# Optimization experiments

Measured on AMD Instinct MI355X. Metric: run time of the kernel, lower is better.

The kernel has to match this reference:

```python
import jax, jax.numpy as jnp
import numpy as np

N = 100000      # nodes
E = 1600000     # edges (avg degree 16)
IN_DIM = 128
OUT_DIM = 64


def setup_inputs() -> dict:
    key = jax.random.key(0)
    k0, k1, k2, k3, k4 = jax.random.split(key, 5)
    h = jax.random.normal(k0, (N, IN_DIM), dtype=jnp.float32)
    src = jax.random.randint(k1, (E,), 0, N)
    dst = jax.random.randint(k2, (E,), 0, N)
    W = jax.random.normal(k3, (OUT_DIM, IN_DIM), dtype=jnp.float32) * 0.05  # fc.weight
    a = jax.random.normal(k4, (2 * OUT_DIM,), dtype=jnp.float32) * 0.05     # attn_fc.weight (flattened)
    return {"h": h, "src": src, "dst": dst, "W": W, "a": a}


def reference(h, src, dst, W, a):
    # z = fc(h)
    z = h @ W.T                                   # [N, OUT_DIM]
    # attn_fc([z_src, z_dst]) == z_src @ a[:D] + z_dst @ a[D:]  (exact linear split)
    s_src = z @ a[:OUT_DIM]                       # [N]
    s_dst = z @ a[OUT_DIM:]                       # [N]
    e = jax.nn.leaky_relu(s_src[src] + s_dst[dst], negative_slope=0.01)  # [E]
    # segment softmax over incoming edges of each dst node
    m = jax.ops.segment_max(e, dst, num_segments=N)
    m = jnp.where(jnp.isfinite(m), m, 0.0)        # empty segments -> -inf; neutralize
    ee = jnp.exp(e - m[dst])                      # [E]
    denom = jax.ops.segment_sum(ee, dst, num_segments=N)
    alpha = ee / jnp.where(denom == 0, 1.0, denom)[dst]
    # scatter-weighted sum of source features
    h_out = jax.ops.segment_sum(alpha[:, None] * z[src], dst, num_segments=N)  # [N, OUT_DIM]
    # activation = F.elu; residual disabled (in_dim != out_dim * num_heads)
    return jax.nn.elu(h_out)
```

## Files before the change

### kernel.cpp

```cpp
#include <hip/hip_runtime.h>
#include <hip/hip_bf16.h>
#include <math.h>

typedef float floatx4 __attribute__((ext_vector_type(4)));
typedef short short8 __attribute__((ext_vector_type(8)));

#define IN_DIM 128
#define OUT_DIM 64
#define OWNER(d) (((d) >> 4) & 7)
#define CHUNK 2048
#define CAP 32
#define OVF_CAP 8192
#define WPAD 136
#define NBIN 512
#define NB_SHIFT 8
#define CELL_CAP 18
#define SPILL_BIT (1 << 20)

__device__ __forceinline__ unsigned short bf16_rne(float f) {
    unsigned u = __float_as_uint(f);
    u += 0x7FFFu + ((u >> 16) & 1u);
    return (unsigned short)(u >> 16);
}
__device__ __forceinline__ float bf16_tof(unsigned short b) {
    return __uint_as_float(((unsigned)b) << 16);
}

__global__ __launch_bounds__(256) void k_gemm(
    const float* __restrict__ h, const float* __restrict__ W,
    const float* __restrict__ a, __hip_bfloat16* __restrict__ z,
    float* __restrict__ s_src, float* __restrict__ s_dst, int N,
    int* __restrict__ meta, int mcount)
{
    __shared__ __align__(16) unsigned short sWhi[64 * WPAD];
    __shared__ __align__(16) unsigned short sWlo[64 * WPAD];

    const int tid = threadIdx.x;
    for (int i = blockIdx.x * 256 + tid; i < mcount; i += gridDim.x * 256)
        meta[i] = 0;

#pragma unroll
    for (int i = 0; i < 32; ++i) {
        int g = tid + 256 * i;
        float f = W[g];
        int row = g >> 7, k = g & 127;
        unsigned short hb = bf16_rne(f);
        sWhi[row * WPAD + k] = hb;
        sWlo[row * WPAD + k] = bf16_rne(f - bf16_tof(hb));
    }

    const int wave = tid >> 6;
    const int l = tid & 63;
    const int lr = l & 15;
    const int lk = l >> 4;
    const int n0w = blockIdx.x * 64 + wave * 16;

    const int arow = min(n0w + lr, N - 1);
    const float* hrow = h + (size_t)arow * IN_DIM;
    short8 ahi[4], alo[4];
#pragma unroll
    for (int ks = 0; ks < 4; ++ks) {
        int k0 = 32 * ks + 8 * lk;
        floatx4 f0 = *(const floatx4*)(hrow + k0);
        floatx4 f1 = *(const floatx4*)(hrow + k0 + 4);
        float fv[8] = {f0.x, f0.y, f0.z, f0.w, f1.x, f1.y, f1.z, f1.w};
#pragma unroll
        for (int j = 0; j < 8; ++j) {
            unsigned short hb = bf16_rne(fv[j]);
            ahi[ks][j] = (short)hb;
            alo[ks][j] = (short)bf16_rne(fv[j] - bf16_tof(hb));
        }
    }
    __syncthreads();

    float ps[4] = {0.f, 0.f, 0.f, 0.f};
    float pd[4] = {0.f, 0.f, 0.f, 0.f};
#pragma unroll
    for (int ct = 0; ct < 4; ++ct) {
        floatx4 acc = (floatx4){0.f, 0.f, 0.f, 0.f};
#pragma unroll
        for (int ks = 0; ks < 4; ++ks) {
            const int boff = (ct * 16 + lr) * WPAD + 32 * ks + 8 * lk;
            short8 bhi = *(const short8*)&sWhi[boff];
            short8 blo = *(const short8*)&sWlo[boff];
            acc = __builtin_amdgcn_mfma_f32_16x16x32_bf16(ahi[ks], bhi, acc, 0, 0, 0);
            acc = __builtin_amdgcn_mfma_f32_16x16x32_bf16(alo[ks], bhi, acc, 0, 0, 0);
            acc = __builtin_amdgcn_mfma_f32_16x16x32_bf16(ahi[ks], blo, acc, 0, 0, 0);
        }
        const float asv = a[ct * 16 + lr];
        const float adv = a[OUT_DIM + ct * 16 + lr];
#pragma unroll
        for (int r = 0; r < 4; ++r) {
            int n = n0w + lk * 4 + r;
            if (n < N)
                z[(size_t)n * OUT_DIM + ct * 16 + lr] = __float2bfloat16(acc[r]);
            ps[r] += acc[r] * asv;
            pd[r] += acc[r] * adv;
        }
    }
#pragma unroll
    for (int r = 0; r < 4; ++r) {
#pragma unroll
        for (int off = 1; off <= 8; off <<= 1) {
            ps[r] += __shfl_xor(ps[r], off);
            pd[r] += __shfl_xor(pd[r], off);
        }
        int n = n0w + lk * 4 + r;
        if (lr == 0 && n < N) {
            s_src[n] = ps[r];
            s_dst[n] = pd[r];
        }
    }
}

__global__ __launch_bounds__(256) void k_bin(
    const int* __restrict__ src, const int* __restrict__ dst,
    int* __restrict__ cursor, unsigned* __restrict__ bdata,
    int* __restrict__ bcnt, int* __restrict__ ovfcnt,
    int2* __restrict__ ovf, int E, int NB, int epb)
{
    __shared__ int cell[512];
    const int tid = threadIdx.x;
    for (int i = tid; i < NB; i += 256) cell[i] = 0;
    __syncthreads();

    const int c = blockIdx.x;
    const int e0 = c * epb;
    const int e1 = min(e0 + epb, E);
    const size_t cbase = (size_t)c * NB * CELL_CAP;
    for (int e = e0 + tid; e < e1; e += 256) {
        int d = __builtin_nontemporal_load(&dst[e]);
        int s = __builtin_nontemporal_load(&src[e]);
        int b = d >> NB_SHIFT;
        int slot = atomicAdd(&cell[b], 1);
        if (slot < CELL_CAP) {
            bdata[cbase + (size_t)b * CELL_CAP + slot] =
                ((unsigned)s << NB_SHIFT) |
                (unsigned)(d & ((1 << NB_SHIFT) - 1));
        } else {
            atomicAdd(&cursor[d], SPILL_BIT);
            int op = atomicAdd(ovfcnt, 1);
            if (op < OVF_CAP) ovf[op] = make_int2(s, d);
        }
    }
    __syncthreads();
    for (int b = tid; b < NB; b += 256) bcnt[c * NB + b] = cell[b];
}

__global__ __launch_bounds__(256) void k_fill(
    const unsigned* __restrict__ bdata, const int* __restrict__ bcnt,
    int* __restrict__ cursor, int* __restrict__ ssort,
    int* __restrict__ ovfcnt, int2* __restrict__ ovf,
    int nb1, int NB, int N)
{
    __shared__ int lcur[256];
    const int tid = threadIdx.x;
    lcur[tid] = 0;
    __syncthreads();

    const int b = blockIdx.x;
    const int n0 = b << NB_SHIFT;
    for (int c = tid; c < nb1; c += 256) {
        int cnt = min(bcnt[c * NB + b], CELL_CAP);
        size_t base = ((size_t)c * NB + b) * CELL_CAP;
        for (int j = 0; j < cnt; ++j) {
            unsigned v = bdata[base + j];
            int i = (int)(v & ((1u << NB_SHIFT) - 1));
            int s = (int)(v >> NB_SHIFT);
            int slot = atomicAdd(&lcur[i], 1);
            if (slot < CAP) {
                ssort[(n0 + i) * CAP + slot] = s;
            } else {
                int op = atomicAdd(ovfcnt, 1);
                if (op < OVF_CAP) ovf[op] = make_int2(s, n0 + i);
            }
        }
    }
    __syncthreads();
    int n = n0 + tid;
    if (n < N) {
        int v = lcur[tid];
        if (v) cursor[n] += v;
    }
}

__global__ __launch_bounds__(256) void k_scatter(
    const int* __restrict__ src, const int* __restrict__ dst,
    int* __restrict__ cursor, int* __restrict__ ssort,
    int* __restrict__ ovfcnt, int2* __restrict__ ovf, int E)
{
    const int x = blockIdx.x & 7;
    const int c = blockIdx.x >> 3;
    const int e0 = c * CHUNK;
#pragma unroll
    for (int i = 0; i < CHUNK / 256; ++i) {
        int e = e0 + i * 256 + threadIdx.x;
        if (e < E) {
            int d = __builtin_nontemporal_load(&dst[e]);
            if (OWNER(d) == x) {
                int s = __builtin_nontemporal_load(&src[e]);
                int pos = atomicAdd(&cursor[d], 1);
                if (pos < CAP) {
                    ssort[d * CAP + pos] = s;
                } else {
                    int op = atomicAdd(ovfcnt, 1);
                    if (op < OVF_CAP) ovf[op] = make_int2(s, d);
                }
            }
        }
    }
}

__global__ __launch_bounds__(256) void k_node(
    const int* __restrict__ cursor, const int* __restrict__ ssort,
    const float* __restrict__ s_src, const float* __restrict__ s_dst,
    const int* __restrict__ ovfcnt, const int2* __restrict__ ovf,
    const __hip_bfloat16* __restrict__ z, float* __restrict__ out, int N)
{
    const int lane = threadIdx.x & 63;
    const int wave = threadIdx.x >> 6;
    const int n = blockIdx.x * 4 + wave;
    if (n >= N) return;

    const int lg = lane >> 4;
    const int lc = lane & 15;

    const int raw = cursor[n];
    if (raw == 0) {
        if (lg == 0) {
            floatx4 zero = (floatx4){0.f, 0.f, 0.f, 0.f};
            __builtin_nontemporal_store(zero, (floatx4*)&out[(size_t)n * OUT_DIM + 4 * lc]);
        }
        return;
    }
    const int low = raw & 0xFFFFF;
    const int deg = min(low, CAP);
    const int base = n * CAP;
    const float sdn = s_dst[n];

    float sum = 0.f;
    int sv = 0;
    float ev = 0.f;
    {
        int kk = lane;
        if (kk < deg) {
            sv = __builtin_nontemporal_load(&ssort[base + kk]);
            float sc = s_src[sv] + sdn;
            sc = sc > 0.f ? sc : 0.01f * sc;
            ev = __expf(sc);
        }
        sum += ev;
    }

    floatx4 acc = (floatx4){0.f, 0.f, 0.f, 0.f};
    for (int j = 0; j < deg; j += 8) {
        int jj0 = j + lg, jj1 = j + 4 + lg;
        bool ok0 = jj0 < deg, ok1 = jj1 < deg;
        int s0 = __shfl(sv, ok0 ? jj0 : 0);
        int s1 = __shfl(sv, ok1 ? jj1 : 0);
        float w0 = __shfl(ev, ok0 ? jj0 : 0);
        float w1 = __shfl(ev, ok1 ? jj1 : 0);
        w0 = ok0 ? w0 : 0.f;
        w1 = ok1 ? w1 : 0.f;
        int sa0 = ok0 ? s0 : 0;
        int sa1 = ok1 ? s1 : 0;
        uint2 v0 = *(const uint2*)&z[(size_t)sa0 * OUT_DIM + 4 * lc];
        uint2 v1 = *(const uint2*)&z[(size_t)sa1 * OUT_DIM + 4 * lc];
        acc.x += w0 * __uint_as_float(v0.x << 16);
        acc.y += w0 * __uint_as_float(v0.x & 0xFFFF0000u);
        acc.z += w0 * __uint_as_float(v0.y << 16);
        acc.w += w0 * __uint_as_float(v0.y & 0xFFFF0000u);
        acc.x += w1 * __uint_as_float(v1.x << 16);
        acc.y += w1 * __uint_as_float(v1.x & 0xFFFF0000u);
        acc.z += w1 * __uint_as_float(v1.y << 16);
        acc.w += w1 * __uint_as_float(v1.y & 0xFFFF0000u);
    }
    acc.x += __shfl_xor(acc.x, 16); acc.y += __shfl_xor(acc.y, 16);
    acc.z += __shfl_xor(acc.z, 16); acc.w += __shfl_xor(acc.w, 16);
    acc.x += __shfl_xor(acc.x, 32); acc.y += __shfl_xor(acc.y, 32);
    acc.z += __shfl_xor(acc.z, 32); acc.w += __shfl_xor(acc.w, 32);

    if (raw > CAP) {
        int oc = min(*ovfcnt, OVF_CAP);
        for (int i = 0; i < oc; ++i) {
            int2 p = ovf[i];
            if (p.y == n) {
                float sc = s_src[p.x] + sdn;
                sc = sc > 0.f ? sc : 0.01f * sc;
                float e2 = __expf(sc);
                if (lane == 0) sum += e2;
                uint2 v = *(const uint2*)&z[(size_t)p.x * OUT_DIM + 4 * lc];
                acc.x += e2 * __uint_as_float(v.x << 16);
                acc.y += e2 * __uint_as_float(v.x & 0xFFFF0000u);
                acc.z += e2 * __uint_as_float(v.y << 16);
                acc.w += e2 * __uint_as_float(v.y & 0xFFFF0000u);
            }
        }
    }

#pragma unroll
    for (int off = 32; off >= 1; off >>= 1) sum += __shfl_xor(sum, off);

    if (lg == 0) {
        float inv = 1.f / sum;
        floatx4 o;
        o.x = acc.x * inv; o.y = acc.y * inv;
        o.z = acc.z * inv; o.w = acc.w * inv;
        o.x = o.x > 0.f ? o.x : __expf(o.x) - 1.f;
        o.y = o.y > 0.f ? o.y : __expf(o.y) - 1.f;
        o.z = o.z > 0.f ? o.z : __expf(o.z) - 1.f;
        o.w = o.w > 0.f ? o.w : __expf(o.w) - 1.f;
        __builtin_nontemporal_store(o, (floatx4*)&out[(size_t)n * OUT_DIM + 4 * lc]);
    }
}

extern "C" void kernel_launch(void* const* d_in, const int* in_sizes, int n_in,
                              void* d_out, int out_size, void* d_ws, size_t ws_size,
                              hipStream_t stream)
{
    (void)n_in; (void)out_size;

    const float* h  = (const float*)d_in[0];
    const int* src  = (const int*)d_in[1];
    const int* dst  = (const int*)d_in[2];
    const float* W  = (const float*)d_in[3];
    const float* a  = (const float*)d_in[4];
    const int N = in_sizes[0] / IN_DIM;
    const int E = in_sizes[1];
    float* out = (float*)d_out;

    const int NB  = (N + (1 << NB_SHIFT) - 1) >> NB_SHIFT;
    const int nb1 = NBIN;
    const int epb = (E + NBIN - 1) / NBIN;

    auto rnd = [](size_t b) { return (b + 255) & ~(size_t)255; };
    const size_t meta_ints = (size_t)N + 1 + (size_t)nb1 * NB;
    const size_t need_bucket =
        rnd((size_t)N * OUT_DIM * 2) + 2 * rnd((size_t)N * 4) +
        rnd(meta_ints * 4) + rnd((size_t)OVF_CAP * 8) +
        rnd((size_t)N * CAP * 4) + rnd((size_t)nb1 * NB * CELL_CAP * 4);
    const bool bucketed = (NB <= 512) && (need_bucket <= ws_size);

    char* wsp = (char*)d_ws;
    size_t off = 0;
    auto alloc = [&](size_t bytes) -> void* {
        void* p = wsp + off;
        off = (off + bytes + 255) & ~(size_t)255;
        return p;
    };
    __hip_bfloat16* z = (__hip_bfloat16*)alloc((size_t)N * OUT_DIM * 2);
    float* s_src = (float*)alloc((size_t)N * 4);
    float* s_dst = (float*)alloc((size_t)N * 4);

    if (bucketed) {
        int* cursor = (int*)alloc(meta_ints * 4);
        int* ovfcnt = cursor + N;
        int* bcnt   = cursor + N + 1;
        int2* ovf   = (int2*)alloc((size_t)OVF_CAP * 8);
        int* ssort  = (int*)alloc((size_t)N * CAP * 4);
        unsigned* bdata = (unsigned*)alloc((size_t)nb1 * NB * CELL_CAP * 4);

        k_gemm<<<(N + 63) / 64, 256, 0, stream>>>(h, W, a, z, s_src, s_dst, N,
                                                  cursor, N + 1);
        k_bin<<<nb1, 256, 0, stream>>>(src, dst, cursor, bdata, bcnt,
                                       ovfcnt, ovf, E, NB, epb);
        k_fill<<<NB, 256, 0, stream>>>(bdata, bcnt, cursor, ssort,
                                       ovfcnt, ovf, nb1, NB, N);
        k_node<<<(N + 3) / 4, 256, 0, stream>>>(cursor, ssort, s_src, s_dst,
                                                ovfcnt, ovf, z, out, N);
    } else {
        int* cursor = (int*)alloc((size_t)(N + 1) * 4);
        int* ovfcnt = cursor + N;
        int2* ovf   = (int2*)alloc((size_t)OVF_CAP * 8);
        int* ssort  = (int*)alloc((size_t)N * CAP * 4);

        const int nchunks = (E + CHUNK - 1) / CHUNK;
        k_gemm<<<(N + 63) / 64, 256, 0, stream>>>(h, W, a, z, s_src, s_dst, N,
                                                  cursor, N + 1);
        k_scatter<<<nchunks * 8, 256, 0, stream>>>(src, dst, cursor, ssort,
                                                   ovfcnt, ovf, E);
        k_node<<<(N + 3) / 4, 256, 0, stream>>>(cursor, ssort, s_src, s_dst,
                                                ovfcnt, ovf, z, out, N);
    }
}
```

Baseline: 212.1 us.

## Merge GEMM and edge binning into one launch to run concurrently

Combines the projection GEMM and the edge-binning pass into a single kernel, where the first NBIN blocks do binning and the remaining blocks do the GEMM. The independent memory-bound binning and compute-bound GEMM can then overlap on the GPU and one launch is removed. The cursor/overflow counter zeroing moves from inside the GEMM kernel to a hipMemsetAsync, which adds a separate memset operation. The fused kernel carries the GEMM's large shared-memory footprint for the binning blocks too, which may lower their occupancy.

```diff
diff --git a/kernel.cpp b/kernel.cpp
--- a/kernel.cpp
+++ b/kernel.cpp
@@ -26,24 +26,58 @@
     return __uint_as_float(((unsigned)b) << 16);
 }
 
-__global__ __launch_bounds__(256) void k_gemm(
+__global__ __launch_bounds__(256) void k_front(
     const float* __restrict__ h, const float* __restrict__ W,
     const float* __restrict__ a, __hip_bfloat16* __restrict__ z,
-    float* __restrict__ s_src, float* __restrict__ s_dst, int N,
-    int* __restrict__ meta, int mcount)
+    float* __restrict__ s_src, float* __restrict__ s_dst, int N, int nG,
+    const int* __restrict__ src, const int* __restrict__ dst,
+    int* __restrict__ cursor, unsigned* __restrict__ bdata,
+    int* __restrict__ bcnt, int* __restrict__ ovfcnt,
+    int2* __restrict__ ovf, int E, int NB, int epb)
 {
     __shared__ __align__(16) unsigned short sWhi[64 * WPAD];
     __shared__ __align__(16) unsigned short sWlo[64 * WPAD];
+    __shared__ int cell[512];
 
     const int tid = threadIdx.x;
-    for (int i = blockIdx.x * 256 + tid; i < mcount; i += gridDim.x * 256)
-        meta[i] = 0;
+    const int b = blockIdx.x;
+
+    if (b < NBIN) {
+        for (int i = tid; i < NB; i += 256) cell[i] = 0;
+        __syncthreads();
+
+        const int c = b;
+        const int e0 = c * epb;
+        const int e1 = min(e0 + epb, E);
+        const size_t cbase = (size_t)c * NB * CELL_CAP;
+        for (int e = e0 + tid; e < e1; e += 256) {
+            int d = __builtin_nontemporal_load(&dst[e]);
+            int s = __builtin_nontemporal_load(&src[e]);
+            int bk = d >> NB_SHIFT;
+            int slot = atomicAdd(&cell[bk], 1);
+            if (slot < CELL_CAP) {
+                bdata[cbase + (size_t)bk * CELL_CAP + slot] =
+                    ((unsigned)s << NB_SHIFT) |
+                    (unsigned)(d & ((1 << NB_SHIFT) - 1));
+            } else {
+                atomicAdd(&cursor[d], SPILL_BIT);
+                int op = atomicAdd(ovfcnt, 1);
+                if (op < OVF_CAP) ovf[op] = make_int2(s, d);
+            }
+        }
+        __syncthreads();
+        for (int bk = tid; bk < NB; bk += 256) bcnt[c * NB + bk] = cell[bk];
+        return;
+    }
+
+    const int g = b - NBIN;
+    if (g >= nG) return;
 
 #pragma unroll
     for (int i = 0; i < 32; ++i) {
-        int g = tid + 256 * i;
-        float f = W[g];
-        int row = g >> 7, k = g & 127;
+        int gg = tid + 256 * i;
+        float f = W[gg];
+        int row = gg >> 7, k = gg & 127;
         unsigned short hb = bf16_rne(f);
         sWhi[row * WPAD + k] = hb;
         sWlo[row * WPAD + k] = bf16_rne(f - bf16_tof(hb));
@@ -53,7 +87,7 @@
     const int l = tid & 63;
     const int lr = l & 15;
     const int lk = l >> 4;
-    const int n0w = blockIdx.x * 64 + wave * 16;
+    const int n0w = g * 64 + wave * 16;
 
     const int arow = min(n0w + lr, N - 1);
     const float* hrow = h + (size_t)arow * IN_DIM;
@@ -111,40 +145,6 @@
             s_dst[n] = pd[r];
         }
     }
-}
-
-__global__ __launch_bounds__(256) void k_bin(
-    const int* __restrict__ src, const int* __restrict__ dst,
-    int* __restrict__ cursor, unsigned* __restrict__ bdata,
-    int* __restrict__ bcnt, int* __restrict__ ovfcnt,
-    int2* __restrict__ ovf, int E, int NB, int epb)
-{
-    __shared__ int cell[512];
-    const int tid = threadIdx.x;
-    for (int i = tid; i < NB; i += 256) cell[i] = 0;
-    __syncthreads();
-
-    const int c = blockIdx.x;
-    const int e0 = c * epb;
-    const int e1 = min(e0 + epb, E);
-    const size_t cbase = (size_t)c * NB * CELL_CAP;
-    for (int e = e0 + tid; e < e1; e += 256) {
-        int d = __builtin_nontemporal_load(&dst[e]);
-        int s = __builtin_nontemporal_load(&src[e]);
-        int b = d >> NB_SHIFT;
-        int slot = atomicAdd(&cell[b], 1);
-        if (slot < CELL_CAP) {
-            bdata[cbase + (size_t)b * CELL_CAP + slot] =
-                ((unsigned)s << NB_SHIFT) |
-                (unsigned)(d & ((1 << NB_SHIFT) - 1));
-        } else {
-            atomicAdd(&cursor[d], SPILL_BIT);
-            int op = atomicAdd(ovfcnt, 1);
-            if (op < OVF_CAP) ovf[op] = make_int2(s, d);
-        }
-    }
-    __syncthreads();
-    for (int b = tid; b < NB; b += 256) bcnt[c * NB + b] = cell[b];
 }
 
 __global__ __launch_bounds__(256) void k_fill(
@@ -181,6 +181,89 @@
     if (n < N) {
         int v = lcur[tid];
         if (v) cursor[n] += v;
+    }
+}
+
+__global__ __launch_bounds__(256) void k_gemm(
+    const float* __restrict__ h, const float* __restrict__ W,
+    const float* __restrict__ a, __hip_bfloat16* __restrict__ z,
+    float* __restrict__ s_src, float* __restrict__ s_dst, int N)
+{
+    __shared__ __align__(16) unsigned short sWhi[64 * WPAD];
+    __shared__ __align__(16) unsigned short sWlo[64 * WPAD];
+
+    const int tid = threadIdx.x;
+#pragma unroll
+    for (int i = 0; i < 32; ++i) {
+        int g = tid + 256 * i;
+        float f = W[g];
+        int row = g >> 7, k = g & 127;
+        unsigned short hb = bf16_rne(f);
+        sWhi[row * WPAD + k] = hb;
+        sWlo[row * WPAD + k] = bf16_rne(f - bf16_tof(hb));
+    }
+
+    const int wave = tid >> 6;
+    const int l = tid & 63;
+    const int lr = l & 15;
+    const int lk = l >> 4;
+    const int n0w = blockIdx.x * 64 + wave * 16;
+
+    const int arow = min(n0w + lr, N - 1);
+    const float* hrow = h + (size_t)arow * IN_DIM;
+    short8 ahi[4], alo[4];
+#pragma unroll
+    for (int ks = 0; ks < 4; ++ks) {
+        int k0 = 32 * ks + 8 * lk;
+        floatx4 f0 = *(const floatx4*)(hrow + k0);
+        floatx4 f1 = *(const floatx4*)(hrow + k0 + 4);
+        float fv[8] = {f0.x, f0.y, f0.z, f0.w, f1.x, f1.y, f1.z, f1.w};
+#pragma unroll
+        for (int j = 0; j < 8; ++j) {
+            unsigned short hb = bf16_rne(fv[j]);
+            ahi[ks][j] = (short)hb;
+            alo[ks][j] = (short)bf16_rne(fv[j] - bf16_tof(hb));
+        }
+    }
+    __syncthreads();
+
+    float ps[4] = {0.f, 0.f, 0.f, 0.f};
+    float pd[4] = {0.f, 0.f, 0.f, 0.f};
+#pragma unroll
+    for (int ct = 0; ct < 4; ++ct) {
+        floatx4 acc = (floatx4){0.f, 0.f, 0.f, 0.f};
+#pragma unroll
+        for (int ks = 0; ks < 4; ++ks) {
+            const int boff = (ct * 16 + lr) * WPAD + 32 * ks + 8 * lk;
+            short8 bhi = *(const short8*)&sWhi[boff];
+            short8 blo = *(const short8*)&sWlo[boff];
+            acc = __builtin_amdgcn_mfma_f32_16x16x32_bf16(ahi[ks], bhi, acc, 0, 0, 0);
+            acc = __builtin_amdgcn_mfma_f32_16x16x32_bf16(alo[ks], bhi, acc, 0, 0, 0);
+            acc = __builtin_amdgcn_mfma_f32_16x16x32_bf16(ahi[ks], blo, acc, 0, 0, 0);
+        }
+        const float asv = a[ct * 16 + lr];
+        const float adv = a[OUT_DIM + ct * 16 + lr];
+#pragma unroll
+        for (int r = 0; r < 4; ++r) {
+            int n = n0w + lk * 4 + r;
+            if (n < N)
+                z[(size_t)n * OUT_DIM + ct * 16 + lr] = __float2bfloat16(acc[r]);
+            ps[r] += acc[r] * asv;
+            pd[r] += acc[r] * adv;
+        }
+    }
+#pragma unroll
+    for (int r = 0; r < 4; ++r) {
+#pragma unroll
+        for (int off = 1; off <= 8; off <<= 1) {
+            ps[r] += __shfl_xor(ps[r], off);
+            pd[r] += __shfl_xor(pd[r], off);
+        }
+        int n = n0w + lk * 4 + r;
+        if (lr == 0 && n < N) {
+            s_src[n] = ps[r];
+            s_dst[n] = pd[r];
+        }
     }
 }
 
@@ -332,6 +415,7 @@
     const int NB  = (N + (1 << NB_SHIFT) - 1) >> NB_SHIFT;
     const int nb1 = NBIN;
     const int epb = (E + NBIN - 1) / NBIN;
+    const int nG  = (N + 63) / 64;
 
     auto rnd = [](size_t b) { return (b + 255) & ~(size_t)255; };
     const size_t meta_ints = (size_t)N + 1 + (size_t)nb1 * NB;
@@ -360,10 +444,10 @@
         int* ssort  = (int*)alloc((size_t)N * CAP * 4);
         unsigned* bdata = (unsigned*)alloc((size_t)nb1 * NB * CELL_CAP * 4);
 
-        k_gemm<<<(N + 63) / 64, 256, 0, stream>>>(h, W, a, z, s_src, s_dst, N,
-                                                  cursor, N + 1);
-        k_bin<<<nb1, 256, 0, stream>>>(src, dst, cursor, bdata, bcnt,
-                                       ovfcnt, ovf, E, NB, epb);
+        hipMemsetAsync(cursor, 0, (size_t)(N + 1) * 4, stream);
+        k_front<<<NBIN + nG, 256, 0, stream>>>(h, W, a, z, s_src, s_dst, N, nG,
+                                               src, dst, cursor, bdata, bcnt,
+                                               ovfcnt, ovf, E, NB, epb);
         k_fill<<<NB, 256, 0, stream>>>(bdata, bcnt, cursor, ssort,
                                        ovfcnt, ovf, nb1, NB, N);
         k_node<<<(N + 3) / 4, 256, 0, stream>>>(cursor, ssort, s_src, s_dst,
@@ -375,8 +459,8 @@
         int* ssort  = (int*)alloc((size_t)N * CAP * 4);
 
         const int nchunks = (E + CHUNK - 1) / CHUNK;
-        k_gemm<<<(N + 63) / 64, 256, 0, stream>>>(h, W, a, z, s_src, s_dst, N,
-                                                  cursor, N + 1);
+        hipMemsetAsync(cursor, 0, (size_t)(N + 1) * 4, stream);
+        k_gemm<<<nG, 256, 0, stream>>>(h, W, a, z, s_src, s_dst, N);
         k_scatter<<<nchunks * 8, 256, 0, stream>>>(src, dst, cursor, ssort,
                                                    ovfcnt, ovf, E);
         k_node<<<(N + 3) / 4, 256, 0, stream>>>(cursor, ssort, s_src, s_dst,
```

Measured after the change: 215.9 us. No clear change (+1.8%).
